# Kernel optimization log

Hardware: AMD Instinct MI355X
Metric: run time of the kernel (lower is better)

Reference implementation:

```python
import jax, jax.numpy as jnp
import numpy as np

NUM_HEADS = 8
KERNEL = 7
LOW_RANK = 4


def setup_inputs() -> dict:
    key = jax.random.key(0)
    ks = jax.random.split(key, 10)
    B, H, W, C = 4, 56, 56, 256
    nh, K, lr = NUM_HEADS, KERNEL, LOW_RANK
    s = 0.02
    return {
        "x": jax.random.normal(ks[0], (B, H, W, C), jnp.float32),
        "Wq": jax.random.normal(ks[1], (C, nh * lr), jnp.float32) * s,
        "bq": jnp.zeros((nh * lr,), jnp.float32),
        "Wk": jax.random.normal(ks[2], (C, nh * lr), jnp.float32) * s,
        "bk": jnp.zeros((nh * lr,), jnp.float32),
        "Wv": jax.random.normal(ks[3], (C, C), jnp.float32) * s,
        "bv": jnp.zeros((C,), jnp.float32),
        "rpb": jax.random.normal(ks[4], (nh, 2 * K - 1, 2 * K - 1), jnp.float32) * s,
        "Wp": jax.random.normal(ks[5], (C, C), jnp.float32) * s,
        "bp": jnp.zeros((C,), jnp.float32),
    }


def reference(x, Wq, bq, Wk, bk, Wv, bv, rpb, Wp, bp):
    B, H, W, C = x.shape
    nh, K, lr = NUM_HEADS, KERNEL, LOW_RANK
    hd = C // nh
    r = K // 2
    scale = hd ** -0.5

    # Projections. Note: the original uses a raw reshape (B,H,W,nh*lr)->(B,nh,H,W,lr),
    # which we replicate exactly (row-major reshape, no permute).
    q = (x @ Wq + bq).reshape(B, nh, H, W, lr) * scale
    k = (x @ Wk + bk).reshape(B, nh, H, W, lr)
    v = (x @ Wv + bv).reshape(B, nh, H, W, hd)

    # NATTEN window start indices (clamped so each query sees exactly K keys per axis).
    start_h = jnp.clip(jnp.arange(H) - r, 0, H - K)  # (H,)
    start_w = jnp.clip(jnp.arange(W) - r, 0, W - K)  # (W,)
    idx_h = start_h[:, None] + jnp.arange(K)[None, :]  # (H, K)
    idx_w = start_w[:, None] + jnp.arange(K)[None, :]  # (W, K)

    # Gather local K/V windows: (B, nh, H, K, W, K, d)
    k_win = k[:, :, idx_h][:, :, :, :, idx_w]
    v_win = v[:, :, idx_h][:, :, :, :, idx_w]

    # Scores: (B, nh, H, W, K, K)
    attn = jnp.einsum('bhijc,bhikjlc->bhijkl', q, k_win)

    # Relative position bias indices: (key_pos - query_pos) + (K-1)
    bi = idx_h - jnp.arange(H)[:, None] + (K - 1)  # (H, K)
    bj = idx_w - jnp.arange(W)[:, None] + (K - 1)  # (W, K)
    bias = rpb[:, bi][:, :, :, bj]                 # (nh, H, K, W, K)
    attn = attn + bias.transpose(0, 1, 3, 2, 4)[None]  # (B, nh, H, W, K, K)

    attn = jax.nn.softmax(attn.reshape(B, nh, H, W, K * K), axis=-1)
    attn = attn.reshape(B, nh, H, W, K, K)

    # Weighted aggregation of V windows: (B, nh, H, W, hd)
    out = jnp.einsum('bhijkl,bhikjld->bhijd', attn, v_win)
    out = out.transpose(0, 2, 3, 1, 4).reshape(B, H, W, C)
    return out @ Wp + bp
```

## Files before the change

kernel.cpp:

```cpp
#include <hip/hip_runtime.h>
#include <hip/hip_bf16.h>

#define BD 4
#define HD_ 56
#define WD 56
#define CD 256
#define NH 8
#define KW 7
#define LR 4
#define HDIM 32
#define MB (HD_*WD)
#define NROWS (BD*MB)
#define QK_PER_B (HD_*WD*32)
#define V_PER_B  (HD_*WD*256)

typedef short short8 __attribute__((ext_vector_type(8)));
typedef float floatx4 __attribute__((ext_vector_type(4)));

static __device__ inline ushort f2bf(float f) {
    __hip_bfloat16 h = __float2bfloat16(f);
    return *(ushort*)&h;
}
static __device__ inline float bf2f(uint h16) {
    union { uint u; float f; } c; c.u = h16 << 16; return c.f;
}
static __device__ inline float bf2f_hi(uint u) {
    union { uint v; float f; } c; c.v = u & 0xffff0000u; return c.f;
}

typedef const __attribute__((address_space(1))) void* gp1_t;
typedef __attribute__((address_space(3))) void* sp3_t;
static __device__ __forceinline__ void glds16(const void* g, void* s) {
    __builtin_amdgcn_global_load_lds((gp1_t)g, (sp3_t)s, 16, 0, 0);
}

__global__ __launch_bounds__(256) void prep_all(
    const float* __restrict__ x,
    const float* __restrict__ Wq, const float* __restrict__ Wk,
    const float* __restrict__ Wv, const float* __restrict__ bq,
    const float* __restrict__ bk, const float* __restrict__ bv,
    const float* __restrict__ Wp,
    ushort* __restrict__ xb, ushort* __restrict__ WpkT,
    ushort* __restrict__ WpT, float* __restrict__ pb)
{
    int idx = blockIdx.x * 256 + threadIdx.x;
    if (idx < 401408) {
        float4 f0 = *(const float4*)&x[idx * 8];
        float4 f1 = *(const float4*)&x[idx * 8 + 4];
        union { ushort h[8]; uint4 u; } p;
        p.h[0] = f2bf(f0.x); p.h[1] = f2bf(f0.y); p.h[2] = f2bf(f0.z); p.h[3] = f2bf(f0.w);
        p.h[4] = f2bf(f1.x); p.h[5] = f2bf(f1.y); p.h[6] = f2bf(f1.z); p.h[7] = f2bf(f1.w);
        *(uint4*)&xb[idx * 8] = p.u;
    } else if (idx < 401408 + 81920) {
        int j = idx - 401408;
        int n = j >> 8, k = j & 255;
        float v;
        if (n < 32)       v = Wq[k * 32 + n];
        else if (n < 64)  v = Wk[k * 32 + (n - 32)];
        else              v = Wv[k * 256 + (n - 64)];
        WpkT[j] = f2bf(v);
    } else if (idx < 401408 + 81920 + 65536) {
        int j = idx - (401408 + 81920);
        int n = j >> 8, k = j & 255;
        WpT[j] = f2bf(Wp[k * 256 + n]);
    } else if (idx < 401408 + 81920 + 65536 + 320) {
        int n = idx - (401408 + 81920 + 65536);
        pb[n] = (n < 32) ? bq[n] : (n < 64) ? bk[n - 32] : bv[n - 64];
    }
}

static __device__ __forceinline__ void gemm_core_128x64(
    const ushort* __restrict__ Ag, const ushort* __restrict__ Bg,
    ushort* As, ushort* Bs, int m0, int n0, int t, floatx4 (&acc)[4][2])
{
    const int lane = t & 63, w = t >> 6;
    const int lx = lane & 7, ly = lane >> 3;
    const int koff = (lx ^ ly) << 3;
    const int col = lane & 15, quad = lane >> 4;
    const int swz = (col & 7) << 4;
    const int wm = w >> 1, wn = w & 1;
    char* Ac = (char*)As;
    char* Bc = (char*)Bs;

    for (int k0 = 0; k0 < 256; k0 += 64) {
        __syncthreads();
#pragma unroll
        for (int l = 0; l < 4; ++l) {
            int c = (w << 2) + l;
            int row = (c << 3) + ly;
            glds16(&Ag[(m0 + row) * 256 + k0 + koff], &As[c << 9]);
        }
#pragma unroll
        for (int l = 0; l < 2; ++l) {
            int c = (w << 1) + l;
            int row = (c << 3) + ly;
            glds16(&Bg[(n0 + row) * 256 + k0 + koff], &Bs[c << 9]);
        }
        __syncthreads();
#pragma unroll
        for (int kk = 0; kk < 2; ++kk) {
            const int kx = ((kk << 6) + (quad << 4)) ^ swz;
            short8 b0 = *(short8*)(Bc + ((wn << 5) + col) * 128 + kx);
            short8 b1 = *(short8*)(Bc + ((wn << 5) + 16 + col) * 128 + kx);
#pragma unroll
            for (int mt = 0; mt < 4; ++mt) {
                short8 a = *(short8*)(Ac + ((wm << 6) + (mt << 4) + col) * 128 + kx);
                acc[mt][0] = __builtin_amdgcn_mfma_f32_16x16x32_bf16(a, b0, acc[mt][0], 0, 0, 0);
                acc[mt][1] = __builtin_amdgcn_mfma_f32_16x16x32_bf16(a, b1, acc[mt][1], 0, 0, 0);
            }
        }
    }
}

__global__ __launch_bounds__(256) void mfma_qkv(
    const ushort* __restrict__ xb, const ushort* __restrict__ Bt,
    const float* __restrict__ pb, ushort* __restrict__ Qb,
    ushort* __restrict__ Kb, ushort* __restrict__ Vb)
{
    __shared__ ushort As[128 * 64];
    __shared__ ushort Bs[64 * 64];
    const int t = threadIdx.x;
    const int m0 = blockIdx.y * 128, n0 = blockIdx.x * 64;

    floatx4 acc[4][2] = {};
    gemm_core_128x64(xb, Bt, As, Bs, m0, n0, t, acc);

    const int lane = t & 63, w = t >> 6;
    const int col = lane & 15, quad = lane >> 4;
    const int wm = w >> 1, wn = w & 1;
#pragma unroll
    for (int mt = 0; mt < 4; ++mt) {
#pragma unroll
        for (int nt = 0; nt < 2; ++nt) {
            int gn = n0 + (wn << 5) + (nt << 4) + col;
            float bias = pb[gn];
#pragma unroll
            for (int rg = 0; rg < 4; ++rg) {
                int m = m0 + (wm << 6) + (mt << 4) + (quad << 2) + rg;
                ushort h = f2bf(acc[mt][nt][rg] + bias);
                if (gn < 32)        Qb[m * 32 + gn] = h;
                else if (gn < 64)   Kb[m * 32 + (gn - 32)] = h;
                else                Vb[m * 256 + (gn - 64)] = h;
            }
        }
    }
}

__global__ __launch_bounds__(256) void natten_attn4(
    const ushort* __restrict__ Qb, const ushort* __restrict__ Kb,
    const ushort* __restrict__ Vb, const float* __restrict__ rpb,
    ushort* __restrict__ Ab)
{
    __shared__ __align__(16) ushort Pl[32 * 168];
    __shared__ __align__(16) ushort Vt[32 * 168];
    __shared__ float4 Ksf[140];
    __shared__ float  Rs[169];
    __shared__ float  invS[32];

    const int tj = blockIdx.x, ti = blockIdx.y;
    const int h = blockIdx.z & 7, b = blockIdx.z >> 3;
    const int t = threadIdx.x;
    const int i0 = ti * 4, j0 = tj * 8;
    const int rs = min(max(i0 - 3, 0), HD_ - 10);
    const int cs = min(max(j0 - 3, 0), WD - 14);

    const ushort* kb = Kb + (size_t)b * QK_PER_B + h * (HD_ * WD * LR);
    const ushort* vb = Vb + (size_t)b * V_PER_B + h * (HD_ * WD * HDIM);

#pragma unroll
    for (int it = 0; it < 3; ++it) {
        int idx = t + (it << 8);
        if (idx < 672) {
            *(uint4*)&Pl[idx << 3] = make_uint4(0, 0, 0, 0);
            *(uint4*)&Vt[idx << 3] = make_uint4(0, 0, 0, 0);
        }
    }
    __syncthreads();

    if (t < 140) {
        int r = t / 14, c = t % 14;
        uint2 kr = *(const uint2*)&kb[(rs + r) * (WD * LR) + (cs + c) * LR];
        Ksf[t] = make_float4(bf2f(kr.x & 0xffff), bf2f_hi(kr.x),
                             bf2f(kr.y & 0xffff), bf2f_hi(kr.y));
    }
    if (t < 169) Rs[t] = rpb[h * 169 + t];
#pragma unroll
    for (int it = 0; it < 3; ++it) {
        int idx = t + (it << 8);
        if (idx < 560) {
            int oct = idx / 140, pos = idx % 140;
            int r = pos / 14, c = pos % 14;
            union { uint4 u; ushort hh[8]; } vv;
            vv.u = *(const uint4*)&vb[(rs + r) * (WD * HDIM) + (cs + c) * HDIM + oct * 8];
            ushort* cp = &Vt[(oct * 8) * 168 + pos];
#pragma unroll
            for (int e = 0; e < 8; ++e) cp[e * 168] = vv.hh[e];
        }
    }

    const int q  = t >> 3, p = t & 7;
    const int qi = q >> 3, qj = q & 7;
    const int i = i0 + qi, j = j0 + qj;
    uint2 qr2 = *(const uint2*)&Qb[(size_t)b * QK_PER_B + h * (HD_ * WD * LR) + i * (WD * LR) + j * LR];
    __syncthreads();

    const int sh = min(max(i - 3, 0), HD_ - KW);
    const int sw = min(max(j - 3, 0), WD - KW);
    const int oh = sh - rs, ow = sw - cs;
    const int rb0 = (sh - i + 6) * 13 + (sw - j + 6);
    const float scale = 0.17677669529663687f;
    float qx = bf2f(qr2.x & 0xffff) * scale, qy = bf2f_hi(qr2.x) * scale;
    float qz = bf2f(qr2.y & 0xffff) * scale, qw = bf2f_hi(qr2.y) * scale;

    float sum = 0.f;
    if (p < 7) {
        int kpos  = (oh + p) * 14 + ow;
        int rbase = rb0 + p * 13;
        ushort* prow = &Pl[q * 168 + kpos];
#pragma unroll
        for (int kw = 0; kw < 7; ++kw) {
            float4 kf = Ksf[kpos + kw];
            float d = Rs[rbase + kw];
            d = fmaf(qx, kf.x, d);
            d = fmaf(qy, kf.y, d);
            d = fmaf(qz, kf.z, d);
            d = fmaf(qw, kf.w, d);
            float e = __expf(d);
            sum += e;
            prow[kw] = f2bf(e);
        }
    }
    sum += __shfl_xor(sum, 1);
    sum += __shfl_xor(sum, 2);
    sum += __shfl_xor(sum, 4);
    if (p == 0) invS[q] = 1.0f / sum;
    __syncthreads();

    const int lane = t & 63, w = t >> 6;
    const int col = lane & 15, quad = lane >> 4;
    const int wm = w & 1, wn = w >> 1;
    floatx4 acc = {0.f, 0.f, 0.f, 0.f};
    const ushort* arow = &Pl[(wm * 16 + col) * 168];
    const ushort* brow = &Vt[(wn * 16 + col) * 168];
#pragma unroll
    for (int s = 0; s < 5; ++s) {
        int ko = s * 32 + quad * 8;
        short8 a  = *(const short8*)(arow + ko);
        short8 bb = *(const short8*)(brow + ko);
        acc = __builtin_amdgcn_mfma_f32_16x16x32_bf16(a, bb, acc, 0, 0, 0);
    }

#pragma unroll
    for (int rg = 0; rg < 4; ++rg) {
        int qq = wm * 16 + quad * 4 + rg;
        float iv = invS[qq];
        int ii = i0 + (qq >> 3), jj = j0 + (qq & 7);
        Ab[(((b * HD_ + ii) * WD + jj)) * CD + h * HDIM + wn * 16 + col] = f2bf(acc[rg] * iv);
    }
}

__global__ __launch_bounds__(256) void mfma_out64(
    const ushort* __restrict__ Ag, const ushort* __restrict__ Bt,
    const float* __restrict__ bp, float* __restrict__ out)
{
    __shared__ ushort As[64 * 64];
    __shared__ ushort Bs[64 * 64];
    const int t = threadIdx.x;
    const int m0 = blockIdx.y * 64, n0 = blockIdx.x * 64;
    const int lane = t & 63, w = t >> 6;
    const int lx = lane & 7, ly = lane >> 3;
    const int koff = (lx ^ ly) << 3;
    const int col = lane & 15, quad = lane >> 4;
    const int swz = (col & 7) << 4;
    const int wm = w >> 1, wn = w & 1;
    char* Ac = (char*)As;
    char* Bc = (char*)Bs;
    floatx4 acc[2][2] = {};

    for (int k0 = 0; k0 < 256; k0 += 64) {
        __syncthreads();
#pragma unroll
        for (int l = 0; l < 2; ++l) {
            int c = (w << 1) + l;
            int row = (c << 3) + ly;
            glds16(&Ag[(m0 + row) * 256 + k0 + koff], &As[c << 9]);
            glds16(&Bt[(n0 + row) * 256 + k0 + koff], &Bs[c << 9]);
        }
        __syncthreads();
#pragma unroll
        for (int kk = 0; kk < 2; ++kk) {
            const int kx = ((kk << 6) + (quad << 4)) ^ swz;
            short8 b0 = *(short8*)(Bc + ((wn << 5) + col) * 128 + kx);
            short8 b1 = *(short8*)(Bc + ((wn << 5) + 16 + col) * 128 + kx);
#pragma unroll
            for (int mt = 0; mt < 2; ++mt) {
                short8 a = *(short8*)(Ac + ((wm << 5) + (mt << 4) + col) * 128 + kx);
                acc[mt][0] = __builtin_amdgcn_mfma_f32_16x16x32_bf16(a, b0, acc[mt][0], 0, 0, 0);
                acc[mt][1] = __builtin_amdgcn_mfma_f32_16x16x32_bf16(a, b1, acc[mt][1], 0, 0, 0);
            }
        }
    }

#pragma unroll
    for (int mt = 0; mt < 2; ++mt) {
#pragma unroll
        for (int nt = 0; nt < 2; ++nt) {
            int gn = n0 + (wn << 5) + (nt << 4) + col;
            float bias = bp[gn];
#pragma unroll
            for (int rg = 0; rg < 4; ++rg) {
                int m = m0 + (wm << 5) + (mt << 4) + (quad << 2) + rg;
                out[m * 256 + gn] = acc[mt][nt][rg] + bias;
            }
        }
    }
}

extern "C" void kernel_launch(void* const* d_in, const int* in_sizes, int n_in,
                              void* d_out, int out_size, void* d_ws, size_t ws_size,
                              hipStream_t stream) {
    const float* x   = (const float*)d_in[0];
    const float* Wq  = (const float*)d_in[1];
    const float* bq  = (const float*)d_in[2];
    const float* Wk  = (const float*)d_in[3];
    const float* bk  = (const float*)d_in[4];
    const float* Wv  = (const float*)d_in[5];
    const float* bv  = (const float*)d_in[6];
    const float* rpb = (const float*)d_in[7];
    const float* Wp  = (const float*)d_in[8];
    const float* bp  = (const float*)d_in[9];
    float* out = (float*)d_out;

    ushort* WpkT = (ushort*)d_ws;
    ushort* WpT  = WpkT + 81920;
    ushort* Ab   = WpT + 65536;
    ushort* Qb   = Ab + 3211264;
    ushort* Kb   = Qb + BD * QK_PER_B;
    ushort* Vb   = Kb + BD * QK_PER_B;
    ushort* xb   = Vb + BD * V_PER_B;
    float*  pb   = (float*)(xb + 3211264);

    prep_all<<<(549184 + 255) / 256, 256, 0, stream>>>(
        x, Wq, Wk, Wv, bq, bk, bv, Wp, xb, WpkT, WpT, pb);

    mfma_qkv<<<dim3(5, NROWS / 128), 256, 0, stream>>>(xb, WpkT, pb, Qb, Kb, Vb);

    natten_attn4<<<dim3(7, 14, 32), 256, 0, stream>>>(Qb, Kb, Vb, rpb, Ab);

    mfma_out64<<<dim3(4, 196), 256, 0, stream>>>(Ab, WpT, bp, out);
}
```

Baseline: 112.6 us.

## Stage full K extent into LDS at once for QKV and output GEMMs

Both projection GEMMs now load the entire 256-deep K slab of A and B into shared memory in one pass with a single barrier, then run all MFMAs, instead of looping over four K-chunks with two barriers each. The QKV GEMM also drops from 128-row to 64-row tiles, doubling its block count. This removes per-chunk barrier stalls and lets all global loads be in flight together, at the cost of 64 KB of LDS per block, which reduces how many blocks can be resident per CU.

Measured after the change: 113.1 us. About the same (+0.4%).

```diff
diff --git a/kernel.cpp b/kernel.cpp
--- a/kernel.cpp
+++ b/kernel.cpp
@@ -69,42 +69,45 @@
     }
 }
 
-static __device__ __forceinline__ void gemm_core_128x64(
+static __device__ __forceinline__ void gemm_stage_full(
     const ushort* __restrict__ Ag, const ushort* __restrict__ Bg,
-    ushort* As, ushort* Bs, int m0, int n0, int t, floatx4 (&acc)[4][2])
+    ushort (*As)[64 * 64], ushort (*Bs)[64 * 64],
+    int m0, int n0, int t)
 {
     const int lane = t & 63, w = t >> 6;
     const int lx = lane & 7, ly = lane >> 3;
     const int koff = (lx ^ ly) << 3;
+#pragma unroll
+    for (int kb = 0; kb < 4; ++kb) {
+#pragma unroll
+        for (int l = 0; l < 2; ++l) {
+            int c = (w << 1) + l;
+            int row = (c << 3) + ly;
+            glds16(&Ag[(m0 + row) * 256 + (kb << 6) + koff], &As[kb][c << 9]);
+            glds16(&Bg[(n0 + row) * 256 + (kb << 6) + koff], &Bs[kb][c << 9]);
+        }
+    }
+}
+
+static __device__ __forceinline__ void gemm_compute_full(
+    ushort (*As)[64 * 64], ushort (*Bs)[64 * 64], int t, floatx4 (&acc)[2][2])
+{
+    const int lane = t & 63, w = t >> 6;
     const int col = lane & 15, quad = lane >> 4;
     const int swz = (col & 7) << 4;
     const int wm = w >> 1, wn = w & 1;
-    char* Ac = (char*)As;
-    char* Bc = (char*)Bs;
-
-    for (int k0 = 0; k0 < 256; k0 += 64) {
-        __syncthreads();
-#pragma unroll
-        for (int l = 0; l < 4; ++l) {
-            int c = (w << 2) + l;
-            int row = (c << 3) + ly;
-            glds16(&Ag[(m0 + row) * 256 + k0 + koff], &As[c << 9]);
-        }
-#pragma unroll
-        for (int l = 0; l < 2; ++l) {
-            int c = (w << 1) + l;
-            int row = (c << 3) + ly;
-            glds16(&Bg[(n0 + row) * 256 + k0 + koff], &Bs[c << 9]);
-        }
-        __syncthreads();
+#pragma unroll
+    for (int kb = 0; kb < 4; ++kb) {
+        char* Ac = (char*)As[kb];
+        char* Bc = (char*)Bs[kb];
 #pragma unroll
         for (int kk = 0; kk < 2; ++kk) {
             const int kx = ((kk << 6) + (quad << 4)) ^ swz;
             short8 b0 = *(short8*)(Bc + ((wn << 5) + col) * 128 + kx);
             short8 b1 = *(short8*)(Bc + ((wn << 5) + 16 + col) * 128 + kx);
 #pragma unroll
-            for (int mt = 0; mt < 4; ++mt) {
-                short8 a = *(short8*)(Ac + ((wm << 6) + (mt << 4) + col) * 128 + kx);
+            for (int mt = 0; mt < 2; ++mt) {
+                short8 a = *(short8*)(Ac + ((wm << 5) + (mt << 4) + col) * 128 + kx);
                 acc[mt][0] = __builtin_amdgcn_mfma_f32_16x16x32_bf16(a, b0, acc[mt][0], 0, 0, 0);
                 acc[mt][1] = __builtin_amdgcn_mfma_f32_16x16x32_bf16(a, b1, acc[mt][1], 0, 0, 0);
             }
@@ -112,35 +115,71 @@
     }
 }
 
-__global__ __launch_bounds__(256) void mfma_qkv(
+__global__ __launch_bounds__(256) void mfma_qkv64(
     const ushort* __restrict__ xb, const ushort* __restrict__ Bt,
     const float* __restrict__ pb, ushort* __restrict__ Qb,
     ushort* __restrict__ Kb, ushort* __restrict__ Vb)
 {
-    __shared__ ushort As[128 * 64];
-    __shared__ ushort Bs[64 * 64];
+    __shared__ ushort As[4][64 * 64];
+    __shared__ ushort Bs[4][64 * 64];
     const int t = threadIdx.x;
-    const int m0 = blockIdx.y * 128, n0 = blockIdx.x * 64;
-
-    floatx4 acc[4][2] = {};
-    gemm_core_128x64(xb, Bt, As, Bs, m0, n0, t, acc);
+    const int m0 = blockIdx.y * 64, n0 = blockIdx.x * 64;
+
+    gemm_stage_full(xb, Bt, As, Bs, m0, n0, t);
+    __syncthreads();
+
+    floatx4 acc[2][2] = {};
+    gemm_compute_full(As, Bs, t, acc);
 
     const int lane = t & 63, w = t >> 6;
     const int col = lane & 15, quad = lane >> 4;
     const int wm = w >> 1, wn = w & 1;
 #pragma unroll
-    for (int mt = 0; mt < 4; ++mt) {
+    for (int mt = 0; mt < 2; ++mt) {
 #pragma unroll
         for (int nt = 0; nt < 2; ++nt) {
             int gn = n0 + (wn << 5) + (nt << 4) + col;
             float bias = pb[gn];
 #pragma unroll
             for (int rg = 0; rg < 4; ++rg) {
-                int m = m0 + (wm << 6) + (mt << 4) + (quad << 2) + rg;
+                int m = m0 + (wm << 5) + (mt << 4) + (quad << 2) + rg;
                 ushort h = f2bf(acc[mt][nt][rg] + bias);
                 if (gn < 32)        Qb[m * 32 + gn] = h;
                 else if (gn < 64)   Kb[m * 32 + (gn - 32)] = h;
                 else                Vb[m * 256 + (gn - 64)] = h;
+            }
+        }
+    }
+}
+
+__global__ __launch_bounds__(256) void mfma_outF(
+    const ushort* __restrict__ Ag, const ushort* __restrict__ Bt,
+    const float* __restrict__ bp, float* __restrict__ out)
+{
+    __shared__ ushort As[4][64 * 64];
+    __shared__ ushort Bs[4][64 * 64];
+    const int t = threadIdx.x;
+    const int m0 = blockIdx.y * 64, n0 = blockIdx.x * 64;
+
+    gemm_stage_full(Ag, Bt, As, Bs, m0, n0, t);
+    __syncthreads();
+
+    floatx4 acc[2][2] = {};
+    gemm_compute_full(As, Bs, t, acc);
+
+    const int lane = t & 63, w = t >> 6;
+    const int col = lane & 15, quad = lane >> 4;
+    const int wm = w >> 1, wn = w & 1;
+#pragma unroll
+    for (int mt = 0; mt < 2; ++mt) {
+#pragma unroll
+        for (int nt = 0; nt < 2; ++nt) {
+            int gn = n0 + (wn << 5) + (nt << 4) + col;
+            float bias = bp[gn];
+#pragma unroll
+            for (int rg = 0; rg < 4; ++rg) {
+                int m = m0 + (wm << 5) + (mt << 4) + (quad << 2) + rg;
+                out[m * 256 + gn] = acc[mt][nt][rg] + bias;
             }
         }
     }
@@ -256,63 +295,6 @@
         float iv = invS[qq];
         int ii = i0 + (qq >> 3), jj = j0 + (qq & 7);
         Ab[(((b * HD_ + ii) * WD + jj)) * CD + h * HDIM + wn * 16 + col] = f2bf(acc[rg] * iv);
-    }
-}
-
-__global__ __launch_bounds__(256) void mfma_out64(
-    const ushort* __restrict__ Ag, const ushort* __restrict__ Bt,
-    const float* __restrict__ bp, float* __restrict__ out)
-{
-    __shared__ ushort As[64 * 64];
-    __shared__ ushort Bs[64 * 64];
-    const int t = threadIdx.x;
-    const int m0 = blockIdx.y * 64, n0 = blockIdx.x * 64;
-    const int lane = t & 63, w = t >> 6;
-    const int lx = lane & 7, ly = lane >> 3;
-    const int koff = (lx ^ ly) << 3;
-    const int col = lane & 15, quad = lane >> 4;
-    const int swz = (col & 7) << 4;
-    const int wm = w >> 1, wn = w & 1;
-    char* Ac = (char*)As;
-    char* Bc = (char*)Bs;
-    floatx4 acc[2][2] = {};
-
-    for (int k0 = 0; k0 < 256; k0 += 64) {
-        __syncthreads();
-#pragma unroll
-        for (int l = 0; l < 2; ++l) {
-            int c = (w << 1) + l;
-            int row = (c << 3) + ly;
-            glds16(&Ag[(m0 + row) * 256 + k0 + koff], &As[c << 9]);
-            glds16(&Bt[(n0 + row) * 256 + k0 + koff], &Bs[c << 9]);
-        }
-        __syncthreads();
-#pragma unroll
-        for (int kk = 0; kk < 2; ++kk) {
-            const int kx = ((kk << 6) + (quad << 4)) ^ swz;
-            short8 b0 = *(short8*)(Bc + ((wn << 5) + col) * 128 + kx);
-            short8 b1 = *(short8*)(Bc + ((wn << 5) + 16 + col) * 128 + kx);
-#pragma unroll
-            for (int mt = 0; mt < 2; ++mt) {
-                short8 a = *(short8*)(Ac + ((wm << 5) + (mt << 4) + col) * 128 + kx);
-                acc[mt][0] = __builtin_amdgcn_mfma_f32_16x16x32_bf16(a, b0, acc[mt][0], 0, 0, 0);
-                acc[mt][1] = __builtin_amdgcn_mfma_f32_16x16x32_bf16(a, b1, acc[mt][1], 0, 0, 0);
-            }
-        }
-    }
-
-#pragma unroll
-    for (int mt = 0; mt < 2; ++mt) {
-#pragma unroll
-        for (int nt = 0; nt < 2; ++nt) {
-            int gn = n0 + (wn << 5) + (nt << 4) + col;
-            float bias = bp[gn];
-#pragma unroll
-            for (int rg = 0; rg < 4; ++rg) {
-                int m = m0 + (wm << 5) + (mt << 4) + (quad << 2) + rg;
-                out[m * 256 + gn] = acc[mt][nt][rg] + bias;
-            }
-        }
     }
 }
 
@@ -343,9 +325,9 @@
     prep_all<<<(549184 + 255) / 256, 256, 0, stream>>>(
         x, Wq, Wk, Wv, bq, bk, bv, Wp, xb, WpkT, WpT, pb);
 
-    mfma_qkv<<<dim3(5, NROWS / 128), 256, 0, stream>>>(xb, WpkT, pb, Qb, Kb, Vb);
+    mfma_qkv64<<<dim3(5, 196), 256, 0, stream>>>(xb, WpkT, pb, Qb, Kb, Vb);
 
     natten_attn4<<<dim3(7, 14, 32), 256, 0, stream>>>(Qb, Kb, Vb, rpb, Ab);
 
-    mfma_out64<<<dim3(4, 196), 256, 0, stream>>>(Ab, WpT, bp, out);
-}
+    mfma_outF<<<dim3(4, 196), 256, 0, stream>>>(Ab, WpT, bp, out);
+}
```

## Merge four kernels into one cooperative persistent kernel with grid syncs

Applied to the files above, without the earlier changes.

Replaces the four separate launches (prep, QKV GEMM, neighborhood attention, output GEMM) with a single cooperative persistent kernel of 512 blocks. The blocks loop over each stage's tiles and separate the stages with grid-wide barriers, and a union of shared-memory layouts serves all stages. This removes per-launch overhead and the gaps between kernels. In exchange it adds grid-sync cost, caps occupancy at 512 resident blocks, and can leave tiles unevenly spread across blocks (for example 490 QKV tiles on 512 blocks).

Measured after the change: 313.6 us. 178% more time.

```diff
diff --git a/kernel.cpp b/kernel.cpp
--- a/kernel.cpp
+++ b/kernel.cpp
@@ -1,5 +1,8 @@
 #include <hip/hip_runtime.h>
 #include <hip/hip_bf16.h>
+#include <hip/hip_cooperative_groups.h>
+
+namespace cg = cooperative_groups;
 
 #define BD 4
 #define HD_ 56
@@ -13,6 +16,7 @@
 #define NROWS (BD*MB)
 #define QK_PER_B (HD_*WD*32)
 #define V_PER_B  (HD_*WD*256)
+#define GRID_B 512
 
 typedef short short8 __attribute__((ext_vector_type(8)));
 typedef float floatx4 __attribute__((ext_vector_type(4)));
@@ -34,40 +38,19 @@
     __builtin_amdgcn_global_load_lds((gp1_t)g, (sp3_t)s, 16, 0, 0);
 }
 
-__global__ __launch_bounds__(256) void prep_all(
-    const float* __restrict__ x,
-    const float* __restrict__ Wq, const float* __restrict__ Wk,
-    const float* __restrict__ Wv, const float* __restrict__ bq,
-    const float* __restrict__ bk, const float* __restrict__ bv,
-    const float* __restrict__ Wp,
-    ushort* __restrict__ xb, ushort* __restrict__ WpkT,
-    ushort* __restrict__ WpT, float* __restrict__ pb)
-{
-    int idx = blockIdx.x * 256 + threadIdx.x;
-    if (idx < 401408) {
-        float4 f0 = *(const float4*)&x[idx * 8];
-        float4 f1 = *(const float4*)&x[idx * 8 + 4];
-        union { ushort h[8]; uint4 u; } p;
-        p.h[0] = f2bf(f0.x); p.h[1] = f2bf(f0.y); p.h[2] = f2bf(f0.z); p.h[3] = f2bf(f0.w);
-        p.h[4] = f2bf(f1.x); p.h[5] = f2bf(f1.y); p.h[6] = f2bf(f1.z); p.h[7] = f2bf(f1.w);
-        *(uint4*)&xb[idx * 8] = p.u;
-    } else if (idx < 401408 + 81920) {
-        int j = idx - 401408;
-        int n = j >> 8, k = j & 255;
-        float v;
-        if (n < 32)       v = Wq[k * 32 + n];
-        else if (n < 64)  v = Wk[k * 32 + (n - 32)];
-        else              v = Wv[k * 256 + (n - 64)];
-        WpkT[j] = f2bf(v);
-    } else if (idx < 401408 + 81920 + 65536) {
-        int j = idx - (401408 + 81920);
-        int n = j >> 8, k = j & 255;
-        WpT[j] = f2bf(Wp[k * 256 + n]);
-    } else if (idx < 401408 + 81920 + 65536 + 320) {
-        int n = idx - (401408 + 81920 + 65536);
-        pb[n] = (n < 32) ? bq[n] : (n < 64) ? bk[n - 32] : bv[n - 64];
-    }
-}
+struct Params {
+    const float *x, *Wq, *bq, *Wk, *bk, *Wv, *bv, *rpb, *Wp, *bp;
+    ushort *xb, *WpkT, *WpT, *Qb, *Kb, *Vb, *Ab;
+    float *pb;
+    float *out;
+};
+
+union SharedU {
+    struct { ushort As[128 * 64]; ushort Bs[64 * 64]; } g;
+    struct { ushort As[64 * 64];  ushort Bs[64 * 64]; } o;
+    struct { ushort Pl[32 * 168]; ushort Vt[32 * 168];
+             float4 Ksf[140]; float Rs[169]; float invS[32]; } a;
+};
 
 static __device__ __forceinline__ void gemm_core_128x64(
     const ushort* __restrict__ Ag, const ushort* __restrict__ Bg,
@@ -112,205 +95,226 @@
     }
 }
 
-__global__ __launch_bounds__(256) void mfma_qkv(
-    const ushort* __restrict__ xb, const ushort* __restrict__ Bt,
-    const float* __restrict__ pb, ushort* __restrict__ Qb,
-    ushort* __restrict__ Kb, ushort* __restrict__ Vb)
+__global__ __launch_bounds__(256, 2) void mono(Params P)
 {
-    __shared__ ushort As[128 * 64];
-    __shared__ ushort Bs[64 * 64];
+    __shared__ SharedU su;
+    cg::grid_group grid = cg::this_grid();
     const int t = threadIdx.x;
-    const int m0 = blockIdx.y * 128, n0 = blockIdx.x * 64;
-
-    floatx4 acc[4][2] = {};
-    gemm_core_128x64(xb, Bt, As, Bs, m0, n0, t, acc);
-
+    const int bid = blockIdx.x;
     const int lane = t & 63, w = t >> 6;
     const int col = lane & 15, quad = lane >> 4;
-    const int wm = w >> 1, wn = w & 1;
-#pragma unroll
-    for (int mt = 0; mt < 4; ++mt) {
-#pragma unroll
-        for (int nt = 0; nt < 2; ++nt) {
-            int gn = n0 + (wn << 5) + (nt << 4) + col;
-            float bias = pb[gn];
+
+#pragma unroll 1
+    for (int it = 0; it < 5; ++it) {
+        int idx = bid * 256 + t + it * (GRID_B * 256);
+        if (idx < 401408) {
+            float4 f0 = *(const float4*)&P.x[idx * 8];
+            float4 f1 = *(const float4*)&P.x[idx * 8 + 4];
+            union { ushort h[8]; uint4 u; } p;
+            p.h[0] = f2bf(f0.x); p.h[1] = f2bf(f0.y); p.h[2] = f2bf(f0.z); p.h[3] = f2bf(f0.w);
+            p.h[4] = f2bf(f1.x); p.h[5] = f2bf(f1.y); p.h[6] = f2bf(f1.z); p.h[7] = f2bf(f1.w);
+            *(uint4*)&P.xb[idx * 8] = p.u;
+        } else if (idx < 401408 + 81920) {
+            int j = idx - 401408;
+            int n = j >> 8, k = j & 255;
+            float v;
+            if (n < 32)       v = P.Wq[k * 32 + n];
+            else if (n < 64)  v = P.Wk[k * 32 + (n - 32)];
+            else              v = P.Wv[k * 256 + (n - 64)];
+            P.WpkT[j] = f2bf(v);
+        } else if (idx < 401408 + 81920 + 65536) {
+            int j = idx - (401408 + 81920);
+            int n = j >> 8, k = j & 255;
+            P.WpT[j] = f2bf(P.Wp[k * 256 + n]);
+        } else if (idx < 401408 + 81920 + 65536 + 320) {
+            int n = idx - (401408 + 81920 + 65536);
+            P.pb[n] = (n < 32) ? P.bq[n] : (n < 64) ? P.bk[n - 32] : P.bv[n - 64];
+        }
+    }
+    grid.sync();
+
+#pragma unroll 1
+    for (int tile = bid; tile < 490; tile += GRID_B) {
+        int n0 = (tile % 5) * 64, m0 = (tile / 5) * 128;
+        floatx4 acc[4][2] = {};
+        gemm_core_128x64(P.xb, P.WpkT, su.g.As, su.g.Bs, m0, n0, t, acc);
+
+        const int wm = w >> 1, wn = w & 1;
+#pragma unroll
+        for (int mt = 0; mt < 4; ++mt) {
+#pragma unroll
+            for (int nt = 0; nt < 2; ++nt) {
+                int gn = n0 + (wn << 5) + (nt << 4) + col;
+                float bias = P.pb[gn];
+#pragma unroll
+                for (int rg = 0; rg < 4; ++rg) {
+                    int m = m0 + (wm << 6) + (mt << 4) + (quad << 2) + rg;
+                    ushort hh = f2bf(acc[mt][nt][rg] + bias);
+                    if (gn < 32)        P.Qb[m * 32 + gn] = hh;
+                    else if (gn < 64)   P.Kb[m * 32 + (gn - 32)] = hh;
+                    else                P.Vb[m * 256 + (gn - 64)] = hh;
+                }
+            }
+        }
+    }
+    grid.sync();
+
+    {
+        const int q = t >> 3, p = t & 7;
+        const int qi = q >> 3, qj = q & 7;
+        const int wmA = w & 1, wnA = w >> 1;
+        const float scale = 0.17677669529663687f;
+#pragma unroll 1
+        for (int tile = bid; tile < 3136; tile += GRID_B) {
+            const int tj = tile % 7;
+            const int rest = tile / 7;
+            const int ti = rest % 14;
+            const int z  = rest / 14;
+            const int h = z & 7, b = z >> 3;
+            const int i0 = ti * 4, j0 = tj * 8;
+            const int rs = min(max(i0 - 3, 0), HD_ - 10);
+            const int cs = min(max(j0 - 3, 0), WD - 14);
+
+            const ushort* kb = P.Kb + (size_t)b * QK_PER_B + h * (HD_ * WD * LR);
+            const ushort* vb = P.Vb + (size_t)b * V_PER_B + h * (HD_ * WD * HDIM);
+
+#pragma unroll
+            for (int it = 0; it < 3; ++it) {
+                int idx = t + (it << 8);
+                if (idx < 672) {
+                    *(uint4*)&su.a.Pl[idx << 3] = make_uint4(0, 0, 0, 0);
+                    *(uint4*)&su.a.Vt[idx << 3] = make_uint4(0, 0, 0, 0);
+                }
+            }
+            __syncthreads();
+
+            if (t < 140) {
+                int r = t / 14, c = t % 14;
+                uint2 kr = *(const uint2*)&kb[(rs + r) * (WD * LR) + (cs + c) * LR];
+                su.a.Ksf[t] = make_float4(bf2f(kr.x & 0xffff), bf2f_hi(kr.x),
+                                          bf2f(kr.y & 0xffff), bf2f_hi(kr.y));
+            }
+            if (t < 169) su.a.Rs[t] = P.rpb[h * 169 + t];
+#pragma unroll
+            for (int it = 0; it < 3; ++it) {
+                int idx = t + (it << 8);
+                if (idx < 560) {
+                    int oct = idx / 140, pos = idx % 140;
+                    int r = pos / 14, c = pos % 14;
+                    union { uint4 u; ushort hh[8]; } vv;
+                    vv.u = *(const uint4*)&vb[(rs + r) * (WD * HDIM) + (cs + c) * HDIM + oct * 8];
+                    ushort* cp = &su.a.Vt[(oct * 8) * 168 + pos];
+#pragma unroll
+                    for (int e = 0; e < 8; ++e) cp[e * 168] = vv.hh[e];
+                }
+            }
+
+            const int i = i0 + qi, j = j0 + qj;
+            uint2 qr2 = *(const uint2*)&P.Qb[(size_t)b * QK_PER_B + h * (HD_ * WD * LR) + i * (WD * LR) + j * LR];
+            __syncthreads();
+
+            const int sh = min(max(i - 3, 0), HD_ - KW);
+            const int sw = min(max(j - 3, 0), WD - KW);
+            const int oh = sh - rs, ow = sw - cs;
+            const int rb0 = (sh - i + 6) * 13 + (sw - j + 6);
+            float qx = bf2f(qr2.x & 0xffff) * scale, qy = bf2f_hi(qr2.x) * scale;
+            float qz = bf2f(qr2.y & 0xffff) * scale, qw = bf2f_hi(qr2.y) * scale;
+
+            float sum = 0.f;
+            if (p < 7) {
+                int kpos  = (oh + p) * 14 + ow;
+                int rbase = rb0 + p * 13;
+                ushort* prow = &su.a.Pl[q * 168 + kpos];
+#pragma unroll
+                for (int kw = 0; kw < 7; ++kw) {
+                    float4 kf = su.a.Ksf[kpos + kw];
+                    float d = su.a.Rs[rbase + kw];
+                    d = fmaf(qx, kf.x, d);
+                    d = fmaf(qy, kf.y, d);
+                    d = fmaf(qz, kf.z, d);
+                    d = fmaf(qw, kf.w, d);
+                    float e = __expf(d);
+                    sum += e;
+                    prow[kw] = f2bf(e);
+                }
+            }
+            sum += __shfl_xor(sum, 1);
+            sum += __shfl_xor(sum, 2);
+            sum += __shfl_xor(sum, 4);
+            if (p == 0) su.a.invS[q] = 1.0f / sum;
+            __syncthreads();
+
+            floatx4 acc = {0.f, 0.f, 0.f, 0.f};
+            const ushort* arow = &su.a.Pl[(wmA * 16 + col) * 168];
+            const ushort* brow = &su.a.Vt[(wnA * 16 + col) * 168];
+#pragma unroll
+            for (int s = 0; s < 5; ++s) {
+                int ko = s * 32 + quad * 8;
+                short8 a  = *(const short8*)(arow + ko);
+                short8 bb = *(const short8*)(brow + ko);
+                acc = __builtin_amdgcn_mfma_f32_16x16x32_bf16(a, bb, acc, 0, 0, 0);
+            }
+
 #pragma unroll
             for (int rg = 0; rg < 4; ++rg) {
-                int m = m0 + (wm << 6) + (mt << 4) + (quad << 2) + rg;
-                ushort h = f2bf(acc[mt][nt][rg] + bias);
-                if (gn < 32)        Qb[m * 32 + gn] = h;
-                else if (gn < 64)   Kb[m * 32 + (gn - 32)] = h;
-                else                Vb[m * 256 + (gn - 64)] = h;
-            }
-        }
-    }
-}
-
-__global__ __launch_bounds__(256) void natten_attn4(
-    const ushort* __restrict__ Qb, const ushort* __restrict__ Kb,
-    const ushort* __restrict__ Vb, const float* __restrict__ rpb,
-    ushort* __restrict__ Ab)
-{
-    __shared__ __align__(16) ushort Pl[32 * 168];
-    __shared__ __align__(16) ushort Vt[32 * 168];
-    __shared__ float4 Ksf[140];
-    __shared__ float  Rs[169];
-    __shared__ float  invS[32];
-
-    const int tj = blockIdx.x, ti = blockIdx.y;
-    const int h = blockIdx.z & 7, b = blockIdx.z >> 3;
-    const int t = threadIdx.x;
-    const int i0 = ti * 4, j0 = tj * 8;
-    const int rs = min(max(i0 - 3, 0), HD_ - 10);
-    const int cs = min(max(j0 - 3, 0), WD - 14);
-
-    const ushort* kb = Kb + (size_t)b * QK_PER_B + h * (HD_ * WD * LR);
-    const ushort* vb = Vb + (size_t)b * V_PER_B + h * (HD_ * WD * HDIM);
-
-#pragma unroll
-    for (int it = 0; it < 3; ++it) {
-        int idx = t + (it << 8);
-        if (idx < 672) {
-            *(uint4*)&Pl[idx << 3] = make_uint4(0, 0, 0, 0);
-            *(uint4*)&Vt[idx << 3] = make_uint4(0, 0, 0, 0);
-        }
-    }
-    __syncthreads();
-
-    if (t < 140) {
-        int r = t / 14, c = t % 14;
-        uint2 kr = *(const uint2*)&kb[(rs + r) * (WD * LR) + (cs + c) * LR];
-        Ksf[t] = make_float4(bf2f(kr.x & 0xffff), bf2f_hi(kr.x),
-                             bf2f(kr.y & 0xffff), bf2f_hi(kr.y));
-    }
-    if (t < 169) Rs[t] = rpb[h * 169 + t];
-#pragma unroll
-    for (int it = 0; it < 3; ++it) {
-        int idx = t + (it << 8);
-        if (idx < 560) {
-            int oct = idx / 140, pos = idx % 140;
-            int r = pos / 14, c = pos % 14;
-            union { uint4 u; ushort hh[8]; } vv;
-            vv.u = *(const uint4*)&vb[(rs + r) * (WD * HDIM) + (cs + c) * HDIM + oct * 8];
-            ushort* cp = &Vt[(oct * 8) * 168 + pos];
-#pragma unroll
-            for (int e = 0; e < 8; ++e) cp[e * 168] = vv.hh[e];
-        }
-    }
-
-    const int q  = t >> 3, p = t & 7;
-    const int qi = q >> 3, qj = q & 7;
-    const int i = i0 + qi, j = j0 + qj;
-    uint2 qr2 = *(const uint2*)&Qb[(size_t)b * QK_PER_B + h * (HD_ * WD * LR) + i * (WD * LR) + j * LR];
-    __syncthreads();
-
-    const int sh = min(max(i - 3, 0), HD_ - KW);
-    const int sw = min(max(j - 3, 0), WD - KW);
-    const int oh = sh - rs, ow = sw - cs;
-    const int rb0 = (sh - i + 6) * 13 + (sw - j + 6);
-    const float scale = 0.17677669529663687f;
-    float qx = bf2f(qr2.x & 0xffff) * scale, qy = bf2f_hi(qr2.x) * scale;
-    float qz = bf2f(qr2.y & 0xffff) * scale, qw = bf2f_hi(qr2.y) * scale;
-
-    float sum = 0.f;
-    if (p < 7) {
-        int kpos  = (oh + p) * 14 + ow;
-        int rbase = rb0 + p * 13;
-        ushort* prow = &Pl[q * 168 + kpos];
-#pragma unroll
-        for (int kw = 0; kw < 7; ++kw) {
-            float4 kf = Ksf[kpos + kw];
-            float d = Rs[rbase + kw];
-            d = fmaf(qx, kf.x, d);
-            d = fmaf(qy, kf.y, d);
-            d = fmaf(qz, kf.z, d);
-            d = fmaf(qw, kf.w, d);
-            float e = __expf(d);
-            sum += e;
-            prow[kw] = f2bf(e);
-        }
-    }
-    sum += __shfl_xor(sum, 1);
-    sum += __shfl_xor(sum, 2);
-    sum += __shfl_xor(sum, 4);
-    if (p == 0) invS[q] = 1.0f / sum;
-    __syncthreads();
-
-    const int lane = t & 63, w = t >> 6;
-    const int col = lane & 15, quad = lane >> 4;
-    const int wm = w & 1, wn = w >> 1;
-    floatx4 acc = {0.f, 0.f, 0.f, 0.f};
-    const ushort* arow = &Pl[(wm * 16 + col) * 168];
-    const ushort* brow = &Vt[(wn * 16 + col) * 168];
-#pragma unroll
-    for (int s = 0; s < 5; ++s) {
-        int ko = s * 32 + quad * 8;
-        short8 a  = *(const short8*)(arow + ko);
-        short8 bb = *(const short8*)(brow + ko);
-        acc = __builtin_amdgcn_mfma_f32_16x16x32_bf16(a, bb, acc, 0, 0, 0);
-    }
-
-#pragma unroll
-    for (int rg = 0; rg < 4; ++rg) {
-        int qq = wm * 16 + quad * 4 + rg;
-        float iv = invS[qq];
-        int ii = i0 + (qq >> 3), jj = j0 + (qq & 7);
-        Ab[(((b * HD_ + ii) * WD + jj)) * CD + h * HDIM + wn * 16 + col] = f2bf(acc[rg] * iv);
-    }
-}
-
-__global__ __launch_bounds__(256) void mfma_out64(
-    const ushort* __restrict__ Ag, const ushort* __restrict__ Bt,
-    const float* __restrict__ bp, float* __restrict__ out)
-{
-    __shared__ ushort As[64 * 64];
-    __shared__ ushort Bs[64 * 64];
-    const int t = threadIdx.x;
-    const int m0 = blockIdx.y * 64, n0 = blockIdx.x * 64;
-    const int lane = t & 63, w = t >> 6;
-    const int lx = lane & 7, ly = lane >> 3;
-    const int koff = (lx ^ ly) << 3;
-    const int col = lane & 15, quad = lane >> 4;
-    const int swz = (col & 7) << 4;
-    const int wm = w >> 1, wn = w & 1;
-    char* Ac = (char*)As;
-    char* Bc = (char*)Bs;
-    floatx4 acc[2][2] = {};
-
-    for (int k0 = 0; k0 < 256; k0 += 64) {
-        __syncthreads();
-#pragma unroll
-        for (int l = 0; l < 2; ++l) {
-            int c = (w << 1) + l;
-            int row = (c << 3) + ly;
-            glds16(&Ag[(m0 + row) * 256 + k0 + koff], &As[c << 9]);
-            glds16(&Bt[(n0 + row) * 256 + k0 + koff], &Bs[c << 9]);
-        }
-        __syncthreads();
-#pragma unroll
-        for (int kk = 0; kk < 2; ++kk) {
-            const int kx = ((kk << 6) + (quad << 4)) ^ swz;
-            short8 b0 = *(short8*)(Bc + ((wn << 5) + col) * 128 + kx);
-            short8 b1 = *(short8*)(Bc + ((wn << 5) + 16 + col) * 128 + kx);
+                int qq = wmA * 16 + quad * 4 + rg;
+                float iv = su.a.invS[qq];
+                int ii = i0 + (qq >> 3), jj = j0 + (qq & 7);
+                P.Ab[(((b * HD_ + ii) * WD + jj)) * CD + h * HDIM + wnA * 16 + col] = f2bf(acc[rg] * iv);
+            }
+            __syncthreads();
+        }
+    }
+    grid.sync();
+
+    {
+        const int lx = lane & 7, ly = lane >> 3;
+        const int koff = (lx ^ ly) << 3;
+        const int swz = (col & 7) << 4;
+        const int wm = w >> 1, wn = w & 1;
+        char* Ac = (char*)su.o.As;
+        char* Bc = (char*)su.o.Bs;
+#pragma unroll 1
+        for (int tile = bid; tile < 784; tile += GRID_B) {
+            int n0 = (tile % 4) * 64, m0 = (tile / 4) * 64;
+            floatx4 acc[2][2] = {};
+
+            for (int k0 = 0; k0 < 256; k0 += 64) {
+                __syncthreads();
+#pragma unroll
+                for (int l = 0; l < 2; ++l) {
+                    int c = (w << 1) + l;
+                    int row = (c << 3) + ly;
+                    glds16(&P.Ab[(m0 + row) * 256 + k0 + koff], &su.o.As[c << 9]);
+                    glds16(&P.WpT[(n0 + row) * 256 + k0 + koff], &su.o.Bs[c << 9]);
+                }
+                __syncthreads();
+#pragma unroll
+                for (int kk = 0; kk < 2; ++kk) {
+                    const int kx = ((kk << 6) + (quad << 4)) ^ swz;
+                    short8 b0 = *(short8*)(Bc + ((wn << 5) + col) * 128 + kx);
+                    short8 b1 = *(short8*)(Bc + ((wn << 5) + 16 + col) * 128 + kx);
+#pragma unroll
+                    for (int mt = 0; mt < 2; ++mt) {
+                        short8 a = *(short8*)(Ac + ((wm << 5) + (mt << 4) + col) * 128 + kx);
+                        acc[mt][0] = __builtin_amdgcn_mfma_f32_16x16x32_bf16(a, b0, acc[mt][0], 0, 0, 0);
+                        acc[mt][1] = __builtin_amdgcn_mfma_f32_16x16x32_bf16(a, b1, acc[mt][1], 0, 0, 0);
+                    }
+                }
+            }
+
 #pragma unroll
             for (int mt = 0; mt < 2; ++mt) {
-                short8 a = *(short8*)(Ac + ((wm << 5) + (mt << 4) + col) * 128 + kx);
-                acc[mt][0] = __builtin_amdgcn_mfma_f32_16x16x32_bf16(a, b0, acc[mt][0], 0, 0, 0);
-                acc[mt][1] = __builtin_amdgcn_mfma_f32_16x16x32_bf16(a, b1, acc[mt][1], 0, 0, 0);
-            }
-        }
-    }
-
-#pragma unroll
-    for (int mt = 0; mt < 2; ++mt) {
-#pragma unroll
-        for (int nt = 0; nt < 2; ++nt) {
-            int gn = n0 + (wn << 5) + (nt << 4) + col;
-            float bias = bp[gn];
-#pragma unroll
-            for (int rg = 0; rg < 4; ++rg) {
-                int m = m0 + (wm << 5) + (mt << 4) + (quad << 2) + rg;
-                out[m * 256 + gn] = acc[mt][nt][rg] + bias;
+#pragma unroll
+                for (int nt = 0; nt < 2; ++nt) {
+                    int gn = n0 + (wn << 5) + (nt << 4) + col;
+                    float bias = P.bp[gn];
+#pragma unroll
+                    for (int rg = 0; rg < 4; ++rg) {
+                        int m = m0 + (wm << 5) + (mt << 4) + (quad << 2) + rg;
+                        P.out[m * 256 + gn] = acc[mt][nt][rg] + bias;
+                    }
+                }
             }
         }
     }
@@ -319,18 +323,6 @@
 extern "C" void kernel_launch(void* const* d_in, const int* in_sizes, int n_in,
                               void* d_out, int out_size, void* d_ws, size_t ws_size,
                               hipStream_t stream) {
-    const float* x   = (const float*)d_in[0];
-    const float* Wq  = (const float*)d_in[1];
-    const float* bq  = (const float*)d_in[2];
-    const float* Wk  = (const float*)d_in[3];
-    const float* bk  = (const float*)d_in[4];
-    const float* Wv  = (const float*)d_in[5];
-    const float* bv  = (const float*)d_in[6];
-    const float* rpb = (const float*)d_in[7];
-    const float* Wp  = (const float*)d_in[8];
-    const float* bp  = (const float*)d_in[9];
-    float* out = (float*)d_out;
-
     ushort* WpkT = (ushort*)d_ws;
     ushort* WpT  = WpkT + 81920;
     ushort* Ab   = WpT + 65536;
@@ -340,12 +332,23 @@
     ushort* xb   = Vb + BD * V_PER_B;
     float*  pb   = (float*)(xb + 3211264);
 
-    prep_all<<<(549184 + 255) / 256, 256, 0, stream>>>(
-        x, Wq, Wk, Wv, bq, bk, bv, Wp, xb, WpkT, WpT, pb);
-
-    mfma_qkv<<<dim3(5, NROWS / 128), 256, 0, stream>>>(xb, WpkT, pb, Qb, Kb, Vb);
-
-    natten_attn4<<<dim3(7, 14, 32), 256, 0, stream>>>(Qb, Kb, Vb, rpb, Ab);
-
-    mfma_out64<<<dim3(4, 196), 256, 0, stream>>>(Ab, WpT, bp, out);
-}
+    Params P;
+    P.x   = (const float*)d_in[0];
+    P.Wq  = (const float*)d_in[1];
+    P.bq  = (const float*)d_in[2];
+    P.Wk  = (const float*)d_in[3];
+    P.bk  = (const float*)d_in[4];
+    P.Wv  = (const float*)d_in[5];
+    P.bv  = (const float*)d_in[6];
+    P.rpb = (const float*)d_in[7];
+    P.Wp  = (const float*)d_in[8];
+    P.bp  = (const float*)d_in[9];
+    P.xb = xb; P.WpkT = WpkT; P.WpT = WpT;
+    P.Qb = Qb; P.Kb = Kb; P.Vb = Vb; P.Ab = Ab;
+    P.pb = pb;
+    P.out = (float*)d_out;
+
+    void* kargs[] = { (void*)&P };
+    hipLaunchCooperativeKernel((const void*)mono, dim3(GRID_B), dim3(256),
+                               kargs, 0, stream);
+}
```

## Fuse fp32-to-bf16 conversion into QKV GEMM and move Wp transpose into attention

Applied to the files above, without the earlier changes.

Removes the separate prep kernel. The QKV GEMM now loads fp32 x and the weights directly, converts them to bf16 in registers and stores them to LDS, which drops the xb round trip through global memory. The weight loads are strided, scalar and uncoalesced, and every block repeats them, so this is redundant work. The Wp transpose and conversion is folded into the first blocks of the attention kernel, and the async global-to-LDS loads are replaced with register staging.

Result: slower. 122.9 us (+9.2%).

```diff
diff --git a/kernel.cpp b/kernel.cpp
--- a/kernel.cpp
+++ b/kernel.cpp
@@ -34,45 +34,18 @@
     __builtin_amdgcn_global_load_lds((gp1_t)g, (sp3_t)s, 16, 0, 0);
 }
 
-__global__ __launch_bounds__(256) void prep_all(
+__global__ __launch_bounds__(256) void qkv_fused(
     const float* __restrict__ x,
     const float* __restrict__ Wq, const float* __restrict__ Wk,
-    const float* __restrict__ Wv, const float* __restrict__ bq,
-    const float* __restrict__ bk, const float* __restrict__ bv,
-    const float* __restrict__ Wp,
-    ushort* __restrict__ xb, ushort* __restrict__ WpkT,
-    ushort* __restrict__ WpT, float* __restrict__ pb)
+    const float* __restrict__ Wv,
+    const float* __restrict__ bq, const float* __restrict__ bk,
+    const float* __restrict__ bv,
+    ushort* __restrict__ Qb, ushort* __restrict__ Kb, ushort* __restrict__ Vb)
 {
-    int idx = blockIdx.x * 256 + threadIdx.x;
-    if (idx < 401408) {
-        float4 f0 = *(const float4*)&x[idx * 8];
-        float4 f1 = *(const float4*)&x[idx * 8 + 4];
-        union { ushort h[8]; uint4 u; } p;
-        p.h[0] = f2bf(f0.x); p.h[1] = f2bf(f0.y); p.h[2] = f2bf(f0.z); p.h[3] = f2bf(f0.w);
-        p.h[4] = f2bf(f1.x); p.h[5] = f2bf(f1.y); p.h[6] = f2bf(f1.z); p.h[7] = f2bf(f1.w);
-        *(uint4*)&xb[idx * 8] = p.u;
-    } else if (idx < 401408 + 81920) {
-        int j = idx - 401408;
-        int n = j >> 8, k = j & 255;
-        float v;
-        if (n < 32)       v = Wq[k * 32 + n];
-        else if (n < 64)  v = Wk[k * 32 + (n - 32)];
-        else              v = Wv[k * 256 + (n - 64)];
-        WpkT[j] = f2bf(v);
-    } else if (idx < 401408 + 81920 + 65536) {
-        int j = idx - (401408 + 81920);
-        int n = j >> 8, k = j & 255;
-        WpT[j] = f2bf(Wp[k * 256 + n]);
-    } else if (idx < 401408 + 81920 + 65536 + 320) {
-        int n = idx - (401408 + 81920 + 65536);
-        pb[n] = (n < 32) ? bq[n] : (n < 64) ? bk[n - 32] : bv[n - 64];
-    }
-}
-
-static __device__ __forceinline__ void gemm_core_128x64(
-    const ushort* __restrict__ Ag, const ushort* __restrict__ Bg,
-    ushort* As, ushort* Bs, int m0, int n0, int t, floatx4 (&acc)[4][2])
-{
+    __shared__ ushort As[128 * 64];
+    __shared__ ushort Bs[64 * 64];
+    const int t = threadIdx.x;
+    const int m0 = blockIdx.y * 128, n0 = blockIdx.x * 64;
     const int lane = t & 63, w = t >> 6;
     const int lx = lane & 7, ly = lane >> 3;
     const int koff = (lx ^ ly) << 3;
@@ -82,19 +55,46 @@
     char* Ac = (char*)As;
     char* Bc = (char*)Bs;
 
+    floatx4 acc[4][2] = {};
+
     for (int k0 = 0; k0 < 256; k0 += 64) {
+        uint4 areg[4], breg[2];
+#pragma unroll
+        for (int l = 0; l < 4; ++l) {
+            int c = (w << 2) + l, row = (c << 3) + ly;
+            float4 f0 = *(const float4*)&x[(m0 + row) * 256 + k0 + koff];
+            float4 f1 = *(const float4*)&x[(m0 + row) * 256 + k0 + koff + 4];
+            union { ushort h[8]; uint4 u; } pk;
+            pk.h[0] = f2bf(f0.x); pk.h[1] = f2bf(f0.y); pk.h[2] = f2bf(f0.z); pk.h[3] = f2bf(f0.w);
+            pk.h[4] = f2bf(f1.x); pk.h[5] = f2bf(f1.y); pk.h[6] = f2bf(f1.z); pk.h[7] = f2bf(f1.w);
+            areg[l] = pk.u;
+        }
+#pragma unroll
+        for (int l = 0; l < 2; ++l) {
+            int c = (w << 1) + l, nr = (c << 3) + ly;
+            int gn = n0 + nr;
+            union { ushort h[8]; uint4 u; } pk;
+#pragma unroll
+            for (int e = 0; e < 8; ++e) {
+                int k = k0 + koff + e;
+                float v;
+                if (gn < 32)       v = Wq[k * 32 + gn];
+                else if (gn < 64)  v = Wk[k * 32 + (gn - 32)];
+                else               v = Wv[k * 256 + (gn - 64)];
+                pk.h[e] = f2bf(v);
+            }
+            breg[l] = pk.u;
+        }
         __syncthreads();
 #pragma unroll
         for (int l = 0; l < 4; ++l) {
             int c = (w << 2) + l;
-            int row = (c << 3) + ly;
-            glds16(&Ag[(m0 + row) * 256 + k0 + koff], &As[c << 9]);
+            *(uint4*)(Ac + (c << 10) + lane * 16) = areg[l];
         }
 #pragma unroll
         for (int l = 0; l < 2; ++l) {
             int c = (w << 1) + l;
-            int row = (c << 3) + ly;
-            glds16(&Bg[(n0 + row) * 256 + k0 + koff], &Bs[c << 9]);
+            *(uint4*)(Bc + (c << 10) + lane * 16) = breg[l];
         }
         __syncthreads();
 #pragma unroll
@@ -110,30 +110,13 @@
             }
         }
     }
-}
-
-__global__ __launch_bounds__(256) void mfma_qkv(
-    const ushort* __restrict__ xb, const ushort* __restrict__ Bt,
-    const float* __restrict__ pb, ushort* __restrict__ Qb,
-    ushort* __restrict__ Kb, ushort* __restrict__ Vb)
-{
-    __shared__ ushort As[128 * 64];
-    __shared__ ushort Bs[64 * 64];
-    const int t = threadIdx.x;
-    const int m0 = blockIdx.y * 128, n0 = blockIdx.x * 64;
-
-    floatx4 acc[4][2] = {};
-    gemm_core_128x64(xb, Bt, As, Bs, m0, n0, t, acc);
-
-    const int lane = t & 63, w = t >> 6;
-    const int col = lane & 15, quad = lane >> 4;
-    const int wm = w >> 1, wn = w & 1;
+
 #pragma unroll
     for (int mt = 0; mt < 4; ++mt) {
 #pragma unroll
         for (int nt = 0; nt < 2; ++nt) {
             int gn = n0 + (wn << 5) + (nt << 4) + col;
-            float bias = pb[gn];
+            float bias = (gn < 32) ? bq[gn] : (gn < 64) ? bk[gn - 32] : bv[gn - 64];
 #pragma unroll
             for (int rg = 0; rg < 4; ++rg) {
                 int m = m0 + (wm << 6) + (mt << 4) + (quad << 2) + rg;
@@ -149,6 +132,7 @@
 __global__ __launch_bounds__(256) void natten_attn4(
     const ushort* __restrict__ Qb, const ushort* __restrict__ Kb,
     const ushort* __restrict__ Vb, const float* __restrict__ rpb,
+    const float* __restrict__ Wp, ushort* __restrict__ WpT,
     ushort* __restrict__ Ab)
 {
     __shared__ __align__(16) ushort Pl[32 * 168];
@@ -160,6 +144,16 @@
     const int tj = blockIdx.x, ti = blockIdx.y;
     const int h = blockIdx.z & 7, b = blockIdx.z >> 3;
     const int t = threadIdx.x;
+
+    {
+        int fb = tj + 7 * (ti + 14 * blockIdx.z);
+        int idx = fb * 256 + t;
+        if (idx < 65536) {
+            int n = idx >> 8, k = idx & 255;
+            WpT[idx] = f2bf(Wp[k * 256 + n]);
+        }
+    }
+
     const int i0 = ti * 4, j0 = tj * 8;
     const int rs = min(max(i0 - 3, 0), HD_ - 10);
     const int cs = min(max(j0 - 3, 0), WD - 14);
@@ -331,21 +325,17 @@
     const float* bp  = (const float*)d_in[9];
     float* out = (float*)d_out;
 
-    ushort* WpkT = (ushort*)d_ws;
-    ushort* WpT  = WpkT + 81920;
-    ushort* Ab   = WpT + 65536;
-    ushort* Qb   = Ab + 3211264;
-    ushort* Kb   = Qb + BD * QK_PER_B;
-    ushort* Vb   = Kb + BD * QK_PER_B;
-    ushort* xb   = Vb + BD * V_PER_B;
-    float*  pb   = (float*)(xb + 3211264);
-
-    prep_all<<<(549184 + 255) / 256, 256, 0, stream>>>(
-        x, Wq, Wk, Wv, bq, bk, bv, Wp, xb, WpkT, WpT, pb);
-
-    mfma_qkv<<<dim3(5, NROWS / 128), 256, 0, stream>>>(xb, WpkT, pb, Qb, Kb, Vb);
-
-    natten_attn4<<<dim3(7, 14, 32), 256, 0, stream>>>(Qb, Kb, Vb, rpb, Ab);
+    ushort* WpT = (ushort*)d_ws;
+    ushort* Ab  = WpT + 65536;
+    ushort* Qb  = Ab + 3211264;
+    ushort* Kb  = Qb + BD * QK_PER_B;
+    ushort* Vb  = Kb + BD * QK_PER_B;
+
+    qkv_fused<<<dim3(5, NROWS / 128), 256, 0, stream>>>(
+        x, Wq, Wk, Wv, bq, bk, bv, Qb, Kb, Vb);
+
+    natten_attn4<<<dim3(7, 14, 32), 256, 0, stream>>>(
+        Qb, Kb, Vb, rpb, Wp, WpT, Ab);
 
     mfma_out64<<<dim3(4, 196), 256, 0, stream>>>(Ab, WpT, bp, out);
 }
```
